# Optimization experiments

Measured on AMD Instinct MI355X. Metric: run time of the kernel, lower is better.

Reference implementation:

```python
import jax, jax.numpy as jnp
import numpy as np

N, E, G, B, L = 24576, 98304, 512, 512, 1000
F_IN, H1, C1, C2, HID = 5, 2, 64, 128, 256


def setup_inputs() -> dict:
    key = jax.random.key(0)
    ks = jax.random.split(key, 20)
    rn = lambda k, s: jax.random.normal(k, s, jnp.float32) * 0.1
    return {
        "x": jax.random.normal(ks[0], (N, F_IN), jnp.float32),
        "edge_index": jax.random.randint(ks[1], (2, E), 0, N),
        "batch": jnp.sort(jax.random.randint(ks[2], (N,), 0, G)),
        "protein_seq": jax.random.randint(ks[3], (B, L), 0, 22),
        "W1": rn(ks[4], (F_IN, H1 * C1)), "att_src1": rn(ks[5], (H1, C1)), "att_dst1": rn(ks[6], (H1, C1)), "b1": jnp.zeros((H1 * C1,), jnp.float32),
        "W2": rn(ks[7], (H1 * C1, C2)), "att_src2": rn(ks[8], (1, C2)), "att_dst2": rn(ks[9], (1, C2)), "b2": jnp.zeros((C2,), jnp.float32),
        "Wd": rn(ks[10], (C2, HID)), "bd": jnp.zeros((HID,), jnp.float32),
        "Pe": rn(ks[11], (22, 64)),
        "K1": rn(ks[12], (64, 64, 3)), "bk1": jnp.zeros((64,), jnp.float32),
        "K2": rn(ks[13], (128, 64, 5)), "bk2": jnp.zeros((128,), jnp.float32),
        "Wp": rn(ks[14], (128, HID)), "bp": jnp.zeros((HID,), jnp.float32),
        "Wf1": rn(ks[15], (2 * HID, 128)), "bf1": jnp.zeros((128,), jnp.float32),
        "Wf2": rn(ks[16], (128, 64)), "bf2": jnp.zeros((64,), jnp.float32),
        "Wo": rn(ks[17], (64, 1)), "bo": jnp.zeros((1,), jnp.float32),
    }


def _gat(x, edge_index, W, att_src, att_dst, b, heads, out_ch):
    """PyG GATConv: add self-loops, per-edge LeakyReLU(0.2) scores, segment softmax over dst."""
    n = x.shape[0]
    h = (x @ W).reshape(n, heads, out_ch)
    loop = jnp.arange(n)
    src = jnp.concatenate([edge_index[0], loop])
    dst = jnp.concatenate([edge_index[1], loop])
    a_s = jnp.sum(h * att_src[None], axis=-1)  # [n, H]
    a_d = jnp.sum(h * att_dst[None], axis=-1)
    e = jax.nn.leaky_relu(a_s[src] + a_d[dst], negative_slope=0.2)  # [E+n, H]
    m = jax.ops.segment_max(e, dst, num_segments=n)
    w = jnp.exp(e - m[dst])
    den = jax.ops.segment_sum(w, dst, num_segments=n)
    alpha = w / (den[dst] + 1e-16)
    out = jax.ops.segment_sum(h[src] * alpha[..., None], dst, num_segments=n)
    return out.reshape(n, heads * out_ch) + b


def _conv1d(x, k, pad):  # x: [B,C,L], k: [O,I,K]
    return jax.lax.conv_general_dilated(x, k, (1,), [(pad, pad)], dimension_numbers=("NCH", "OIH", "NCH"))


def reference(x, edge_index, batch, protein_seq, W1, att_src1, att_dst1, b1, W2, att_src2, att_dst2, b2, Wd, bd, Pe, K1, bk1, K2, bk2, Wp, bp, Wf1, bf1, Wf2, bf2, Wo, bo):
    # drug branch (GAT x2 + global mean pool)
    g = jax.nn.elu(_gat(x, edge_index, W1, att_src1, att_dst1, b1, H1, C1))
    g = jax.nn.elu(_gat(g, edge_index, W2, att_src2, att_dst2, b2, 1, C2))
    sums = jax.ops.segment_sum(g, batch, num_segments=G)
    cnt = jax.ops.segment_sum(jnp.ones((g.shape[0], 1), g.dtype), batch, num_segments=G)
    drug = jax.nn.relu(sums / jnp.maximum(cnt, 1.0) @ Wd + bd)
    # protein branch (embed -> conv1d x2 -> global max pool)
    pe = Pe[protein_seq].transpose(0, 2, 1)  # [B, 64, L]
    p = jax.nn.elu(_conv1d(pe, K1, 1) + bk1[None, :, None])
    p = jax.nn.elu(_conv1d(p, K2, 2) + bk2[None, :, None])
    prot = jax.nn.relu(jnp.max(p, axis=2) @ Wp + bp)
    # head
    h = jnp.concatenate([drug, prot], axis=1)
    h = jax.nn.relu(h @ Wf1 + bf1)
    h = jax.nn.relu(h @ Wf2 + bf2)
    return h @ Wo + bo
```

## Files before the change

kernel.cpp:

```cpp
#include <hip/hip_runtime.h>
#include <hip/hip_bf16.h>
#include <math.h>

#define NN 24576
#define NE 98304
#define ETOT (NE + NN)
#define NG 512
#define NB 512
#define LL 1000
#define TL 60
#define NTILE 17
#define PROT_BLKS (NB * NTILE)
#define CNT_BLKS (ETOT / 256)
#define AS1_BLKS (NN * 2 / 256)

typedef __attribute__((ext_vector_type(8))) short short8;
typedef __attribute__((ext_vector_type(4))) short short4v;
typedef __attribute__((ext_vector_type(4))) float f32x4;

__device__ inline short f2bf(float x) {
    union { __hip_bfloat16 b; short s; } u;
    u.b = __float2bfloat16(x);
    return u.s;
}

__device__ inline float bf2f(short s) {
    return __uint_as_float(((unsigned)(unsigned short)s) << 16);
}

__global__ void k_init_prep(int* deg, int* cursor, float* sums, float* cnt,
                            const float* K1, const float* K2, const float* W2, const float* Pe,
                            const float* W1, const float* as1c, const float* ad1c,
                            const float* as2c, const float* ad2c, const float* bk1,
                            short* Bswz2, short* Bh2, short* Bl2, float* M1,
                            float* wvec) {
    int bid = blockIdx.x, t = threadIdx.x;
    if (bid < 256) {
        int i = bid * 256 + t;
        if (i < NN) { deg[i] = 0; cursor[i] = 0; }
        if (i < NG * 128) sums[i] = 0.f;
        if (i < NG) cnt[i] = 0.f;
        return;
    }
    int idx = (bid - 256) * 256 + t;
    if (idx < 20) {
        int q = idx % 10, hd = q / 5, f = q % 5;
        const float* av = (idx < 10) ? as1c : ad1c;
        float s = 0.f;
        for (int c = 0; c < 64; c++) s += W1[f * 128 + hd * 64 + c] * av[hd * 64 + c];
        wvec[idx < 10 ? q : 10 + q] = s;
    }
    if (idx >= 32 && idx < 288) {
        int q = idx - 32;
        int kk = q & 127;
        const float* av = (q < 128) ? as2c : ad2c;
        float s = 0.f;
        for (int n2 = 0; n2 < 128; n2++) s += W2[kk * 128 + n2] * av[n2];
        wvec[idx] = s;
    }
    if (idx < 22 * 3 * 64) {
        int tok = idx / 192, r2 = idx % 192;
        int k = r2 >> 6, oc = r2 & 63;
        float s = (k == 1) ? bk1[oc] : 0.f;
        for (int ic = 0; ic < 64; ic++) s += K1[oc * 192 + ic * 3 + k] * Pe[tok * 64 + ic];
        M1[idx] = s;
    }
    if (idx < 320 * 128) {
        int j = idx & 7, lane = (idx >> 3) & 63, rest = idx >> 9;
        int nt = rest & 7, kb = rest >> 3;
        int k = kb * 32 + ((lane >> 4) << 3) + j;
        int n = nt * 16 + (lane & 15);
        int kk = k / 64, i = k % 64;
        Bswz2[idx] = f2bf(K2[n * 320 + i * 5 + kk]);
    }
    if (idx < 128 * 128) {
        int j = idx & 7, lane = (idx >> 3) & 63, rest = idx >> 9;
        int nt = rest & 7, kb = rest >> 3;
        int k = kb * 32 + ((lane >> 4) << 3) + j;
        int n = nt * 16 + (lane & 15);
        float v = W2[k * 128 + n];
        short hh = f2bf(v);
        Bh2[idx] = hh;
        Bl2[idx] = f2bf(v - bf2f(hh));
    }
}

#define SSTR 72
__global__ __launch_bounds__(256, 6) void k_prot_cnt_as1(
    const int* seq, const float* M1,
    const short* Bswz2, float* pmaxp,
    const int* ei, int* deg, const int* batch, float* cnt,
    const float* x, const float* wvec, float* rec) {
    int bid = blockIdx.x;
    int t = threadIdx.x;

    if (bid < CNT_BLKS) {
        int e = bid * 256 + t;
        int d = (e < NE) ? ei[NE + e] : e - NE;
        atomicAdd(&deg[d], 1);
        return;
    }
    if (bid < CNT_BLKS + AS1_BLKS) {
        int idx = (bid - CNT_BLKS) * 256 + t;
        int n = idx >> 1, hd = idx & 1;
        float xv[5];
        float s = 0.f, dv = 0.f;
#pragma unroll
        for (int f = 0; f < 5; f++) {
            xv[f] = x[n * 5 + f];
            s += xv[f] * wvec[hd * 5 + f];
            dv += xv[f] * wvec[10 + hd * 5 + f];
        }
        float* rr = &rec[n * 16];
        if (hd == 0) {
#pragma unroll
            for (int f = 0; f < 5; f++) rr[f] = xv[f];
            rr[5] = s; rr[7] = dv;
            atomicAdd(&cnt[batch[n]], 1.f);
        } else {
            rr[6] = s; rr[8] = dv;
        }
        return;
    }

    __shared__ __align__(16) short s1[68 * SSTR];

    int pb = bid - (CNT_BLKS + AS1_BLKS);
    int b = pb / NTILE;
    int tile = pb - b * NTILE;
    int t0 = tile * TL;

    if (t < 36) {
        *(short8*)&s1[64 * SSTR + t * 8] = (short8){0, 0, 0, 0, 0, 0, 0, 0};
    }

    {
        int q = t >> 2, c0 = (t & 3) << 4;
        int l = t0 - 2 + q;
        short tmp[16];
        if (l >= 0 && l < LL) {
            float v[16];
#pragma unroll
            for (int j = 0; j < 16; j++) v[j] = 0.f;
#pragma unroll
            for (int k = 0; k < 3; k++) {
                int lp = l - 1 + k;
                if (lp >= 0 && lp < LL) {
                    int tok = seq[b * LL + lp];
                    const float4* mr = (const float4*)&M1[tok * 192 + k * 64 + c0];
#pragma unroll
                    for (int j = 0; j < 4; j++) {
                        float4 mv = mr[j];
                        v[j * 4 + 0] += mv.x; v[j * 4 + 1] += mv.y;
                        v[j * 4 + 2] += mv.z; v[j * 4 + 3] += mv.w;
                    }
                }
            }
#pragma unroll
            for (int j = 0; j < 16; j++) {
                float xv = v[j];
                xv = xv > 0.f ? xv : __expf(xv) - 1.f;
                tmp[j] = f2bf(xv);
            }
        } else {
#pragma unroll
            for (int j = 0; j < 16; j++) tmp[j] = 0;
        }
        *(short8*)&s1[q * SSTR + c0] = *(short8*)&tmp[0];
        *(short8*)&s1[q * SSTR + c0 + 8] = *(short8*)&tmp[8];
    }
    __syncthreads();

    int wv = t >> 6, lane = t & 63;
    int ln15 = lane & 15, quad = lane >> 4;

    f32x4 acc2[4][2];
#pragma unroll
    for (int mi = 0; mi < 4; mi++)
#pragma unroll
        for (int ni = 0; ni < 2; ni++) acc2[mi][ni] = (f32x4){0.f, 0.f, 0.f, 0.f};
#pragma unroll
    for (int kb = 0; kb < 10; kb++) {
        int koff = kb * 32 + quad * 8;
        int kk = koff >> 6, i0 = koff & 63;
        short8 a[4], bb[2];
#pragma unroll
        for (int mi = 0; mi < 4; mi++)
            a[mi] = *(const short8*)&s1[(mi * 16 + ln15 + kk) * SSTR + i0];
#pragma unroll
        for (int ni = 0; ni < 2; ni++)
            bb[ni] = *(const short8*)&Bswz2[((kb * 8 + wv * 2 + ni) * 64 + lane) * 8];
#pragma unroll
        for (int mi = 0; mi < 4; mi++)
#pragma unroll
            for (int ni = 0; ni < 2; ni++)
                acc2[mi][ni] = __builtin_amdgcn_mfma_f32_16x16x32_bf16(a[mi], bb[ni], acc2[mi][ni], 0, 0, 0);
    }

#pragma unroll
    for (int ni = 0; ni < 2; ni++) {
        int col = (wv * 2 + ni) * 16 + ln15;
        float mx = -1e30f;
#pragma unroll
        for (int mi = 0; mi < 4; mi++) {
#pragma unroll
            for (int r = 0; r < 4; r++) {
                int p = mi * 16 + quad * 4 + r;
                if (p < TL && t0 + p < LL) mx = fmaxf(mx, acc2[mi][ni][r]);
            }
        }
        mx = fmaxf(mx, __shfl_xor(mx, 16, 64));
        mx = fmaxf(mx, __shfl_xor(mx, 32, 64));
        if (quad == 0) pmaxp[(b * NTILE + tile) * 128 + col] = mx;
    }
}

__global__ void k_scan1(const int* deg, int* excl, int* part) {
    __shared__ int s[256];
    int b = blockIdx.x, t = threadIdx.x, i = b * 256 + t;
    int v = deg[i];
    s[t] = v;
    __syncthreads();
    for (int o = 1; o < 256; o <<= 1) {
        int x = (t >= o) ? s[t - o] : 0;
        __syncthreads();
        s[t] += x;
        __syncthreads();
    }
    excl[i] = s[t] - v;
    if (t == 255) part[b] = s[t];
}

__global__ void k_scan23(const int* excl, const int* part, int* rowptr) {
    __shared__ int sp[96];
    __shared__ int pref;
    int b = blockIdx.x, t = threadIdx.x;
    if (t < 96) sp[t] = part[t];
    __syncthreads();
    if (t == 0) {
        int run = 0;
        for (int i = 0; i < b; i++) run += sp[i];
        pref = run;
    }
    __syncthreads();
    int i = b * 256 + t;
    rowptr[i] = excl[i] + pref;
    if (i == 0) rowptr[NN] = ETOT;
}

__global__ void k_scatter(const int* ei, const int* rowptr, int* cursor, int* colidx) {
    int e = blockIdx.x * 256 + threadIdx.x;
    if (e >= ETOT) return;
    int s, d;
    if (e < NE) { s = ei[e]; d = ei[NE + e]; }
    else { s = d = e - NE; }
    int pos = atomicAdd(&cursor[d], 1);
    colidx[rowptr[d] + pos] = s;
}

__global__ void k_agg2x(const int* rowptr, const int* colidx, const float* rec,
                        const float* W1, const float* b1, const float* wvec,
                        unsigned int* g1b, float* as2, float* ad2) {
    __shared__ float sW[640];
    __shared__ float sb1[128];
    __shared__ float swa[256];
    int t = threadIdx.x;
    for (int i = t; i < 640; i += 256) sW[i] = W1[i];
    if (t < 128) { sb1[t] = b1[t]; swa[t] = wvec[32 + t]; swa[128 + t] = wvec[160 + t]; }
    __syncthreads();

    int d = blockIdx.x * 16 + (t >> 4);
    int g = t & 15;
    int hd = (g < 5) ? 0 : 1;
    int f = (g < 5) ? g : g - 5;
    float adv = rec[d * 16 + 7 + hd];
    int p0 = rowptr[d], p1 = rowptr[d + 1];
    float den = 0.f, acc = 0.f;
    if (g < 10) {
        for (int pc = p0; pc < p1; pc += 4) {
            int sarr[4]; float ev[4], xv[4];
#pragma unroll
            for (int i = 0; i < 4; i++) {
                int pp = pc + i;
                sarr[i] = colidx[pp < p1 ? pp : p1 - 1];
            }
#pragma unroll
            for (int i = 0; i < 4; i++) {
                ev[i] = rec[sarr[i] * 16 + 5 + hd];
                xv[i] = rec[sarr[i] * 16 + f];
            }
#pragma unroll
            for (int i = 0; i < 4; i++) {
                if (pc + i < p1) {
                    float e = ev[i] + adv;
                    e = e >= 0.f ? e : 0.2f * e;
                    float w = __expf(e);
                    den += w;
                    acc += w * xv[i];
                }
            }
        }
    }
    float xn = acc / (den + 1e-16f);
    int gb = (t & 63) & ~15;
    int hcol = g >> 3;
    float xs[5];
#pragma unroll
    for (int f2 = 0; f2 < 5; f2++)
        xs[f2] = __shfl(xn, gb + hcol * 5 + f2, 64);
    float ps = 0.f, pd = 0.f;
    float g1v[8];
#pragma unroll
    for (int k = 0; k < 8; k++) {
        int col = g * 8 + k;
        float v = sb1[col];
#pragma unroll
        for (int f2 = 0; f2 < 5; f2++) v += xs[f2] * sW[f2 * 128 + col];
        v = v > 0.f ? v : __expf(v) - 1.f;
        g1v[k] = v;
        ps += v * swa[col];
        pd += v * swa[128 + col];
    }
    uint4 pk;
    pk.x = ((unsigned)(unsigned short)f2bf(g1v[1]) << 16) | (unsigned)(unsigned short)f2bf(g1v[0]);
    pk.y = ((unsigned)(unsigned short)f2bf(g1v[3]) << 16) | (unsigned)(unsigned short)f2bf(g1v[2]);
    pk.z = ((unsigned)(unsigned short)f2bf(g1v[5]) << 16) | (unsigned)(unsigned short)f2bf(g1v[4]);
    pk.w = ((unsigned)(unsigned short)f2bf(g1v[7]) << 16) | (unsigned)(unsigned short)f2bf(g1v[6]);
    *(uint4*)&g1b[d * 64 + g * 4] = pk;
#pragma unroll
    for (int msk = 1; msk < 16; msk <<= 1) {
        ps += __shfl_xor(ps, msk, 64);
        pd += __shfl_xor(pd, msk, 64);
    }
    if (g == 0) { as2[d] = ps; ad2[d] = pd; }
}

__global__ void k_agg1y(const int* rowptr, const int* colidx, const unsigned int* hb,
                        const float* as_, const float* ad_, float* yacc) {
    int t = threadIdx.x;
    int d = blockIdx.x * 4 + (t >> 6);
    int c = t & 63;
    float adv = ad_[d];
    int p0 = rowptr[d], p1 = rowptr[d + 1];
    float den = 0.f, acc0 = 0.f, acc1 = 0.f;
    for (int pc = p0; pc < p1; pc += 4) {
        int sarr[4]; float ev[4]; unsigned int hv[4];
#pragma unroll
        for (int i = 0; i < 4; i++) {
            int pp = pc + i;
            sarr[i] = colidx[pp < p1 ? pp : p1 - 1];
        }
#pragma unroll
        for (int i = 0; i < 4; i++) {
            ev[i] = as_[sarr[i]];
            hv[i] = hb[sarr[i] * 64 + c];
        }
#pragma unroll
        for (int i = 0; i < 4; i++) {
            if (pc + i < p1) {
                float e = ev[i] + adv;
                e = e >= 0.f ? e : 0.2f * e;
                float w = __expf(e);
                den += w;
                acc0 += w * __uint_as_float(hv[i] << 16);
                acc1 += w * __uint_as_float(hv[i] & 0xFFFF0000u);
            }
        }
    }
    float inv = 1.f / (den + 1e-16f);
    ((float2*)yacc)[d * 64 + c] = (float2){acc0 * inv, acc1 * inv};
}

#define ASTR 136
__global__ __launch_bounds__(256, 2) void k_g2mm(
    const float* yacc, const short* Bh, const short* Bl, const float* b2,
    const int* batch, float* sums) {
    __shared__ __align__(16) short Ah[64 * ASTR];
    __shared__ __align__(16) short Al[64 * ASTR];
    __shared__ int sb[64];
    int t = threadIdx.x;
    int m0 = blockIdx.x * 64;
    int wv = t >> 6, lane = t & 63;
    int ln15 = lane & 15, quad = lane >> 4;

    if (t < 64) sb[t] = batch[m0 + t];
    for (int i = t; i < 64 * 32; i += 256) {
        int row = i >> 5, c4 = (i & 31) * 4;
        float4 v = *(const float4*)&yacc[(m0 + row) * 128 + c4];
        short4v hi, lo;
        hi.x = f2bf(v.x); lo.x = f2bf(v.x - bf2f(hi.x));
        hi.y = f2bf(v.y); lo.y = f2bf(v.y - bf2f(hi.y));
        hi.z = f2bf(v.z); lo.z = f2bf(v.z - bf2f(hi.z));
        hi.w = f2bf(v.w); lo.w = f2bf(v.w - bf2f(hi.w));
        *(short4v*)&Ah[row * ASTR + c4] = hi;
        *(short4v*)&Al[row * ASTR + c4] = lo;
    }
    __syncthreads();

    f32x4 acc[8];
#pragma unroll
    for (int nt = 0; nt < 8; nt++) acc[nt] = (f32x4){0.f, 0.f, 0.f, 0.f};
    int arow = wv * 16 + ln15;
#pragma unroll
    for (int kb = 0; kb < 4; kb++) {
        int koff = kb * 32 + quad * 8;
        short8 a_hi = *(const short8*)&Ah[arow * ASTR + koff];
        short8 a_lo = *(const short8*)&Al[arow * ASTR + koff];
#pragma unroll
        for (int nt = 0; nt < 8; nt++) {
            short8 bh = *(const short8*)&Bh[((kb * 8 + nt) * 64 + lane) * 8];
            short8 bl = *(const short8*)&Bl[((kb * 8 + nt) * 64 + lane) * 8];
            acc[nt] = __builtin_amdgcn_mfma_f32_16x16x32_bf16(a_hi, bh, acc[nt], 0, 0, 0);
            acc[nt] = __builtin_amdgcn_mfma_f32_16x16x32_bf16(a_hi, bl, acc[nt], 0, 0, 0);
            acc[nt] = __builtin_amdgcn_mfma_f32_16x16x32_bf16(a_lo, bh, acc[nt], 0, 0, 0);
        }
    }
    int rbase = wv * 16 + quad * 4;
#pragma unroll
    for (int nt = 0; nt < 8; nt++) {
        int col = nt * 16 + ln15;
        float bias = b2[col];
        float run = 0.f;
        int cg = sb[rbase];
#pragma unroll
        for (int r = 0; r < 4; r++) {
            float v = acc[nt][r] + bias;
            v = v > 0.f ? v : __expf(v) - 1.f;
            int g = sb[rbase + r];
            if (g != cg) {
                atomicAdd(&sums[cg * 128 + col], run);
                run = 0.f; cg = g;
            }
            run += v;
        }
        atomicAdd(&sums[cg * 128 + col], run);
    }
}

__global__ __launch_bounds__(512) void k_tail(
    const float* pmaxp, const float* bk2, const float* Wp, const float* bp,
    const float* sums, const float* cnt, const float* Wd, const float* bd,
    const float* Wf1, const float* bf1, const float* Wf2, const float* bf2,
    const float* Wo, const float* bo, float* out) {
    __shared__ float spm[128];
    __shared__ float in2[512];
    __shared__ float part1[512];
    __shared__ float hh[128];
    __shared__ float part2[512];
    __shared__ float h2s[64];
    int g = blockIdx.x, t = threadIdx.x;

    if (t < 128) {
        float m = -1e30f;
#pragma unroll
        for (int tt = 0; tt < NTILE; tt++)
            m = fmaxf(m, pmaxp[(g * NTILE + tt) * 128 + t]);
        float v = m + bk2[t];
        spm[t] = v > 0.f ? v : __expf(v) - 1.f;
    }
    __syncthreads();

    if (t < 256) {
        float pacc = bp[t];
#pragma unroll 8
        for (int i = 0; i < 128; i++) pacc += spm[i] * Wp[i * 256 + t];
        in2[256 + t] = pacc > 0.f ? pacc : 0.f;
    } else {
        int o = t - 256;
        float c = cnt[g]; c = c < 1.f ? 1.f : c;
        float inv = 1.f / c;
        float dacc = bd[o];
#pragma unroll 8
        for (int i = 0; i < 128; i++) dacc += sums[g * 128 + i] * inv * Wd[i * 256 + o];
        in2[o] = dacc > 0.f ? dacc : 0.f;
    }
    __syncthreads();

    {
        int o = t >> 2, ks = t & 3;
        float p = 0.f;
        int c0 = ks * 128;
#pragma unroll 8
        for (int cc = c0; cc < c0 + 128; cc++) p += in2[cc] * Wf1[cc * 128 + o];
        part1[t] = p;
    }
    __syncthreads();
    if (t < 128) {
        float a = bf1[t] + part1[t * 4] + part1[t * 4 + 1] + part1[t * 4 + 2] + part1[t * 4 + 3];
        hh[t] = a > 0.f ? a : 0.f;
    }
    __syncthreads();

    {
        int o = t >> 3, ks = t & 7;
        float p = 0.f;
        int c0 = ks * 16;
#pragma unroll
        for (int cc = c0; cc < c0 + 16; cc++) p += hh[cc] * Wf2[cc * 64 + o];
        part2[t] = p;
    }
    __syncthreads();
    if (t < 64) {
        float a = bf2[t];
#pragma unroll
        for (int k = 0; k < 8; k++) a += part2[t * 8 + k];
        h2s[t] = a > 0.f ? a : 0.f;
    }
    __syncthreads();

    if (t < 64) {
        float p = h2s[t] * Wo[t];
#pragma unroll
        for (int off = 32; off > 0; off >>= 1) p += __shfl_down(p, off, 64);
        if (t == 0) out[g] = p + bo[0];
    }
}

extern "C" void kernel_launch(void* const* d_in, const int* in_sizes, int n_in,
                              void* d_out, int out_size, void* d_ws, size_t ws_size,
                              hipStream_t stream) {
    (void)in_sizes; (void)n_in; (void)out_size; (void)ws_size;
    const float* x   = (const float*)d_in[0];
    const int* ei    = (const int*)d_in[1];
    const int* batch = (const int*)d_in[2];
    const int* seq   = (const int*)d_in[3];
    const float* W1  = (const float*)d_in[4];
    const float* a_s1 = (const float*)d_in[5];
    const float* a_d1 = (const float*)d_in[6];
    const float* b1  = (const float*)d_in[7];
    const float* W2  = (const float*)d_in[8];
    const float* a_s2 = (const float*)d_in[9];
    const float* a_d2 = (const float*)d_in[10];
    const float* b2  = (const float*)d_in[11];
    const float* Wd  = (const float*)d_in[12];
    const float* bd  = (const float*)d_in[13];
    const float* Pe  = (const float*)d_in[14];
    const float* K1  = (const float*)d_in[15];
    const float* bk1 = (const float*)d_in[16];
    const float* K2  = (const float*)d_in[17];
    const float* bk2 = (const float*)d_in[18];
    const float* Wp  = (const float*)d_in[19];
    const float* bp  = (const float*)d_in[20];
    const float* Wf1 = (const float*)d_in[21];
    const float* bf1 = (const float*)d_in[22];
    const float* Wf2 = (const float*)d_in[23];
    const float* bf2 = (const float*)d_in[24];
    const float* Wo  = (const float*)d_in[25];
    const float* bo  = (const float*)d_in[26];
    float* out = (float*)d_out;

    float* w = (float*)d_ws;
    float* g1bf = w; w += NN * 64;
    float* yacc = w; w += NN * 128;
    float* as2  = w; w += NN;
    float* ad2  = w; w += NN;
    float* sums = w; w += NG * 128;
    float* cnt  = w; w += NG;
    float* pmaxp = w; w += NB * NTILE * 128;
    float* rec  = w; w += NN * 16;
    float* wvec = w; w += 512;
    short* Bswz2 = (short*)w; w += 320 * 128 / 2;
    short* Bh2  = (short*)w; w += 128 * 128 / 2;
    short* Bl2  = (short*)w; w += 128 * 128 / 2;
    float* M1   = w; w += 22 * 3 * 64;
    int* deg    = (int*)w; w += NN;
    int* cursor = (int*)w; w += NN;
    int* excl   = (int*)w; w += NN;
    int* part   = (int*)w; w += 128;
    int* rowptr = (int*)w; w += NN + 8;
    int* colidx = (int*)w; w += ETOT;

    unsigned int* g1b = (unsigned int*)g1bf;

    hipLaunchKernelGGL(k_init_prep, dim3(256 + 160), dim3(256), 0, stream,
                       deg, cursor, sums, cnt,
                       K1, K2, W2, Pe, W1, a_s1, a_d1, a_s2, a_d2, bk1,
                       Bswz2, Bh2, Bl2, M1, wvec);

    hipLaunchKernelGGL(k_prot_cnt_as1, dim3(CNT_BLKS + AS1_BLKS + PROT_BLKS), dim3(256), 0, stream,
                       seq, M1, Bswz2, pmaxp,
                       ei, deg, batch, cnt, x, wvec, rec);

    hipLaunchKernelGGL(k_scan1, dim3(NN / 256), dim3(256), 0, stream, deg, excl, part);
    hipLaunchKernelGGL(k_scan23, dim3(NN / 256), dim3(256), 0, stream, excl, part, rowptr);
    hipLaunchKernelGGL(k_scatter, dim3(ETOT / 256), dim3(256), 0, stream, ei, rowptr, cursor, colidx);

    hipLaunchKernelGGL(k_agg2x, dim3(NN / 16), dim3(256), 0, stream,
                       rowptr, colidx, rec, W1, b1, wvec, g1b, as2, ad2);

    hipLaunchKernelGGL(k_agg1y, dim3(NN / 4), dim3(256), 0, stream,
                       rowptr, colidx, g1b, as2, ad2, yacc);

    hipLaunchKernelGGL(k_g2mm, dim3(NN / 64), dim3(256), 0, stream,
                       yacc, Bh2, Bl2, b2, batch, sums);

    hipLaunchKernelGGL(k_tail, dim3(NG), dim3(512), 0, stream,
                       pmaxp, bk2, Wp, bp, sums, cnt, Wd, bd, Wf1, bf1, Wf2, bf2, Wo, bo, out);
}
```

Before: 282.6 us.

## Spread protein conv tiles across graph-build kernels and merge scan passes

Splits the 8704 protein conv tiles into four chunks and places them as extra blocks in the degree-count, scan, scatter and first-aggregation kernels. Graph CSR-build kernels have few blocks and leave the GPU underused, so the dense MFMA work is meant to fill those idle compute units. The two scan kernels are merged into one using an atomic counter spin-wait across the 96 scan blocks, which removes a launch and the excl buffer. The spin-wait can deadlock if the scan blocks are not all resident at once, and unroll 2 on the MFMA loop trades instruction count against scheduling freedom.

```diff
diff --git a/kernel.cpp b/kernel.cpp
--- a/kernel.cpp
+++ b/kernel.cpp
@@ -10,9 +10,17 @@
 #define LL 1000
 #define TL 60
 #define NTILE 17
-#define PROT_BLKS (NB * NTILE)
+#define PROT_TOT (NB * NTILE)
 #define CNT_BLKS (ETOT / 256)
 #define AS1_BLKS (NN * 2 / 256)
+#define P1_CNT 1792
+#define P2_CNT 1280
+#define P3_CNT 1536
+#define P4_CNT 4096
+#define P1_OFF 0
+#define P2_OFF (P1_CNT)
+#define P3_OFF (P1_CNT + P2_CNT)
+#define P4_OFF (P1_CNT + P2_CNT + P3_CNT)
 
 typedef __attribute__((ext_vector_type(8))) short short8;
 typedef __attribute__((ext_vector_type(4))) short short4v;
@@ -28,7 +36,101 @@
     return __uint_as_float(((unsigned)(unsigned short)s) << 16);
 }
 
-__global__ void k_init_prep(int* deg, int* cursor, float* sums, float* cnt,
+#define SSTR 72
+#define SMEM_BYTES 9792
+__device__ __forceinline__ void prot_body(int pb, int t, char* smem,
+        const int* seq, const float* M1, const short* Bswz2, float* pmaxp) {
+    short* s1 = (short*)smem;
+    int b = pb / NTILE;
+    int tile = pb - b * NTILE;
+    int t0 = tile * TL;
+
+    if (t < 36) {
+        *(short8*)&s1[64 * SSTR + t * 8] = (short8){0, 0, 0, 0, 0, 0, 0, 0};
+    }
+
+    {
+        int q = t >> 2, c0 = (t & 3) << 4;
+        int l = t0 - 2 + q;
+        short tmp[16];
+        if (l >= 0 && l < LL) {
+            float v[16];
+#pragma unroll
+            for (int j = 0; j < 16; j++) v[j] = 0.f;
+#pragma unroll
+            for (int k = 0; k < 3; k++) {
+                int lp = l - 1 + k;
+                if (lp >= 0 && lp < LL) {
+                    int tok = seq[b * LL + lp];
+                    const float4* mr = (const float4*)&M1[tok * 192 + k * 64 + c0];
+#pragma unroll
+                    for (int j = 0; j < 4; j++) {
+                        float4 mv = mr[j];
+                        v[j * 4 + 0] += mv.x; v[j * 4 + 1] += mv.y;
+                        v[j * 4 + 2] += mv.z; v[j * 4 + 3] += mv.w;
+                    }
+                }
+            }
+#pragma unroll
+            for (int j = 0; j < 16; j++) {
+                float xv = v[j];
+                xv = xv > 0.f ? xv : __expf(xv) - 1.f;
+                tmp[j] = f2bf(xv);
+            }
+        } else {
+#pragma unroll
+            for (int j = 0; j < 16; j++) tmp[j] = 0;
+        }
+        *(short8*)&s1[q * SSTR + c0] = *(short8*)&tmp[0];
+        *(short8*)&s1[q * SSTR + c0 + 8] = *(short8*)&tmp[8];
+    }
+    __syncthreads();
+
+    int wv = t >> 6, lane = t & 63;
+    int ln15 = lane & 15, quad = lane >> 4;
+
+    f32x4 acc2[4][2];
+#pragma unroll
+    for (int mi = 0; mi < 4; mi++)
+#pragma unroll
+        for (int ni = 0; ni < 2; ni++) acc2[mi][ni] = (f32x4){0.f, 0.f, 0.f, 0.f};
+#pragma unroll 2
+    for (int kb = 0; kb < 10; kb++) {
+        int koff = kb * 32 + quad * 8;
+        int kk = koff >> 6, i0 = koff & 63;
+        short8 a[4], bb[2];
+#pragma unroll
+        for (int mi = 0; mi < 4; mi++)
+            a[mi] = *(const short8*)&s1[(mi * 16 + ln15 + kk) * SSTR + i0];
+#pragma unroll
+        for (int ni = 0; ni < 2; ni++)
+            bb[ni] = *(const short8*)&Bswz2[((kb * 8 + wv * 2 + ni) * 64 + lane) * 8];
+#pragma unroll
+        for (int mi = 0; mi < 4; mi++)
+#pragma unroll
+            for (int ni = 0; ni < 2; ni++)
+                acc2[mi][ni] = __builtin_amdgcn_mfma_f32_16x16x32_bf16(a[mi], bb[ni], acc2[mi][ni], 0, 0, 0);
+    }
+
+#pragma unroll
+    for (int ni = 0; ni < 2; ni++) {
+        int col = (wv * 2 + ni) * 16 + ln15;
+        float mx = -1e30f;
+#pragma unroll
+        for (int mi = 0; mi < 4; mi++) {
+#pragma unroll
+            for (int r = 0; r < 4; r++) {
+                int p = mi * 16 + quad * 4 + r;
+                if (p < TL && t0 + p < LL) mx = fmaxf(mx, acc2[mi][ni][r]);
+            }
+        }
+        mx = fmaxf(mx, __shfl_xor(mx, 16, 64));
+        mx = fmaxf(mx, __shfl_xor(mx, 32, 64));
+        if (quad == 0) pmaxp[(b * NTILE + tile) * 128 + col] = mx;
+    }
+}
+
+__global__ void k_init_prep(int* deg, int* cursor, float* sums, float* cnt, int* ctr,
                             const float* K1, const float* K2, const float* W2, const float* Pe,
                             const float* W1, const float* as1c, const float* ad1c,
                             const float* as2c, const float* ad2c, const float* bk1,
@@ -40,6 +142,7 @@
         if (i < NN) { deg[i] = 0; cursor[i] = 0; }
         if (i < NG * 128) sums[i] = 0.f;
         if (i < NG) cnt[i] = 0.f;
+        if (i == 0) ctr[0] = 0;
         return;
     }
     int idx = (bid - 256) * 256 + t;
@@ -85,14 +188,12 @@
     }
 }
 
-#define SSTR 72
-__global__ __launch_bounds__(256, 6) void k_prot_cnt_as1(
-    const int* seq, const float* M1,
-    const short* Bswz2, float* pmaxp,
+__global__ __launch_bounds__(256, 6) void k_d2(
     const int* ei, int* deg, const int* batch, float* cnt,
-    const float* x, const float* wvec, float* rec) {
-    int bid = blockIdx.x;
-    int t = threadIdx.x;
+    const float* x, const float* wvec, float* rec,
+    const int* seq, const float* M1, const short* Bswz2, float* pmaxp) {
+    int bid = blockIdx.x, t = threadIdx.x;
+    __shared__ __align__(16) char smem[SMEM_BYTES];
 
     if (bid < CNT_BLKS) {
         int e = bid * 256 + t;
@@ -122,154 +223,89 @@
         }
         return;
     }
-
-    __shared__ __align__(16) short s1[68 * SSTR];
-
-    int pb = bid - (CNT_BLKS + AS1_BLKS);
-    int b = pb / NTILE;
-    int tile = pb - b * NTILE;
-    int t0 = tile * TL;
-
-    if (t < 36) {
-        *(short8*)&s1[64 * SSTR + t * 8] = (short8){0, 0, 0, 0, 0, 0, 0, 0};
-    }
-
-    {
-        int q = t >> 2, c0 = (t & 3) << 4;
-        int l = t0 - 2 + q;
-        short tmp[16];
-        if (l >= 0 && l < LL) {
-            float v[16];
-#pragma unroll
-            for (int j = 0; j < 16; j++) v[j] = 0.f;
-#pragma unroll
-            for (int k = 0; k < 3; k++) {
-                int lp = l - 1 + k;
-                if (lp >= 0 && lp < LL) {
-                    int tok = seq[b * LL + lp];
-                    const float4* mr = (const float4*)&M1[tok * 192 + k * 64 + c0];
-#pragma unroll
-                    for (int j = 0; j < 4; j++) {
-                        float4 mv = mr[j];
-                        v[j * 4 + 0] += mv.x; v[j * 4 + 1] += mv.y;
-                        v[j * 4 + 2] += mv.z; v[j * 4 + 3] += mv.w;
-                    }
-                }
-            }
-#pragma unroll
-            for (int j = 0; j < 16; j++) {
-                float xv = v[j];
-                xv = xv > 0.f ? xv : __expf(xv) - 1.f;
-                tmp[j] = f2bf(xv);
-            }
-        } else {
-#pragma unroll
-            for (int j = 0; j < 16; j++) tmp[j] = 0;
-        }
-        *(short8*)&s1[q * SSTR + c0] = *(short8*)&tmp[0];
-        *(short8*)&s1[q * SSTR + c0 + 8] = *(short8*)&tmp[8];
-    }
-    __syncthreads();
-
-    int wv = t >> 6, lane = t & 63;
-    int ln15 = lane & 15, quad = lane >> 4;
-
-    f32x4 acc2[4][2];
-#pragma unroll
-    for (int mi = 0; mi < 4; mi++)
-#pragma unroll
-        for (int ni = 0; ni < 2; ni++) acc2[mi][ni] = (f32x4){0.f, 0.f, 0.f, 0.f};
-#pragma unroll
-    for (int kb = 0; kb < 10; kb++) {
-        int koff = kb * 32 + quad * 8;
-        int kk = koff >> 6, i0 = koff & 63;
-        short8 a[4], bb[2];
-#pragma unroll
-        for (int mi = 0; mi < 4; mi++)
-            a[mi] = *(const short8*)&s1[(mi * 16 + ln15 + kk) * SSTR + i0];
-#pragma unroll
-        for (int ni = 0; ni < 2; ni++)
-            bb[ni] = *(const short8*)&Bswz2[((kb * 8 + wv * 2 + ni) * 64 + lane) * 8];
-#pragma unroll
-        for (int mi = 0; mi < 4; mi++)
-#pragma unroll
-            for (int ni = 0; ni < 2; ni++)
-                acc2[mi][ni] = __builtin_amdgcn_mfma_f32_16x16x32_bf16(a[mi], bb[ni], acc2[mi][ni], 0, 0, 0);
-    }
-
-#pragma unroll
-    for (int ni = 0; ni < 2; ni++) {
-        int col = (wv * 2 + ni) * 16 + ln15;
-        float mx = -1e30f;
-#pragma unroll
-        for (int mi = 0; mi < 4; mi++) {
-#pragma unroll
-            for (int r = 0; r < 4; r++) {
-                int p = mi * 16 + quad * 4 + r;
-                if (p < TL && t0 + p < LL) mx = fmaxf(mx, acc2[mi][ni][r]);
-            }
-        }
-        mx = fmaxf(mx, __shfl_xor(mx, 16, 64));
-        mx = fmaxf(mx, __shfl_xor(mx, 32, 64));
-        if (quad == 0) pmaxp[(b * NTILE + tile) * 128 + col] = mx;
-    }
-}
-
-__global__ void k_scan1(const int* deg, int* excl, int* part) {
-    __shared__ int s[256];
-    int b = blockIdx.x, t = threadIdx.x, i = b * 256 + t;
-    int v = deg[i];
-    s[t] = v;
-    __syncthreads();
-    for (int o = 1; o < 256; o <<= 1) {
-        int x = (t >= o) ? s[t - o] : 0;
+    prot_body(P1_OFF + (bid - (CNT_BLKS + AS1_BLKS)), t, smem, seq, M1, Bswz2, pmaxp);
+}
+
+__global__ __launch_bounds__(256, 6) void k_scan(
+    const int* deg, int* rowptr, int* part, int* ctr,
+    const int* seq, const float* M1, const short* Bswz2, float* pmaxp) {
+    int bid = blockIdx.x, t = threadIdx.x;
+    __shared__ __align__(16) char smem[SMEM_BYTES];
+
+    if (bid < 96) {
+        int* s = (int*)smem;
+        int* sp = (int*)(smem + 1024);
+        int b = bid, i = b * 256 + t;
+        int v = deg[i];
+        s[t] = v;
         __syncthreads();
-        s[t] += x;
+        for (int o = 1; o < 256; o <<= 1) {
+            int x2 = (t >= o) ? s[t - o] : 0;
+            __syncthreads();
+            s[t] += x2;
+            __syncthreads();
+        }
+        int excl = s[t] - v;
+        if (t == 255) {
+            part[b] = s[t];
+            __threadfence();
+            atomicAdd(ctr, 1);
+        }
+        if (t == 0) {
+            while (__hip_atomic_load(ctr, __ATOMIC_ACQUIRE, __HIP_MEMORY_SCOPE_AGENT) < 96) {}
+        }
         __syncthreads();
-    }
-    excl[i] = s[t] - v;
-    if (t == 255) part[b] = s[t];
-}
-
-__global__ void k_scan23(const int* excl, const int* part, int* rowptr) {
-    __shared__ int sp[96];
-    __shared__ int pref;
-    int b = blockIdx.x, t = threadIdx.x;
-    if (t < 96) sp[t] = part[t];
-    __syncthreads();
-    if (t == 0) {
-        int run = 0;
-        for (int i = 0; i < b; i++) run += sp[i];
-        pref = run;
-    }
-    __syncthreads();
-    int i = b * 256 + t;
-    rowptr[i] = excl[i] + pref;
-    if (i == 0) rowptr[NN] = ETOT;
-}
-
-__global__ void k_scatter(const int* ei, const int* rowptr, int* cursor, int* colidx) {
-    int e = blockIdx.x * 256 + threadIdx.x;
-    if (e >= ETOT) return;
-    int s, d;
-    if (e < NE) { s = ei[e]; d = ei[NE + e]; }
-    else { s = d = e - NE; }
-    int pos = atomicAdd(&cursor[d], 1);
-    colidx[rowptr[d] + pos] = s;
-}
-
-__global__ void k_agg2x(const int* rowptr, const int* colidx, const float* rec,
-                        const float* W1, const float* b1, const float* wvec,
-                        unsigned int* g1b, float* as2, float* ad2) {
-    __shared__ float sW[640];
-    __shared__ float sb1[128];
-    __shared__ float swa[256];
-    int t = threadIdx.x;
+        if (t < 96) sp[t] = __hip_atomic_load(&part[t], __ATOMIC_RELAXED, __HIP_MEMORY_SCOPE_AGENT);
+        __syncthreads();
+        int pref = 0;
+        for (int i2 = 0; i2 < b; i2++) pref += sp[i2];
+        rowptr[i] = excl + pref;
+        if (i == 0) rowptr[NN] = ETOT;
+        return;
+    }
+    prot_body(P2_OFF + (bid - 96), t, smem, seq, M1, Bswz2, pmaxp);
+}
+
+__global__ __launch_bounds__(256, 6) void k_scat(
+    const int* ei, const int* rowptr, int* cursor, int* colidx,
+    const int* seq, const float* M1, const short* Bswz2, float* pmaxp) {
+    int bid = blockIdx.x, t = threadIdx.x;
+    __shared__ __align__(16) char smem[SMEM_BYTES];
+
+    if (bid < CNT_BLKS) {
+        int e = bid * 256 + t;
+        int s, d;
+        if (e < NE) { s = ei[e]; d = ei[NE + e]; }
+        else { s = d = e - NE; }
+        int pos = atomicAdd(&cursor[d], 1);
+        colidx[rowptr[d] + pos] = s;
+        return;
+    }
+    prot_body(P3_OFF + (bid - CNT_BLKS), t, smem, seq, M1, Bswz2, pmaxp);
+}
+
+__global__ __launch_bounds__(256, 4) void k_mega(
+    const int* rowptr, const int* colidx, const float* rec,
+    const float* W1, const float* b1, const float* wvec,
+    unsigned int* g1b, float* as2, float* ad2,
+    const int* seq, const float* M1, const short* Bswz2, float* pmaxp) {
+    int bid = blockIdx.x, t = threadIdx.x;
+    __shared__ __align__(16) char smem[SMEM_BYTES];
+
+    int grp = bid / 11, r = bid - grp * 11;
+    if (r >= 3) {
+        prot_body(P4_OFF + grp * 8 + (r - 3), t, smem, seq, M1, Bswz2, pmaxp);
+        return;
+    }
+    int a = grp * 3 + r;
+    float* sW = (float*)smem;
+    float* sb1 = sW + 640;
+    float* swa = sb1 + 128;
     for (int i = t; i < 640; i += 256) sW[i] = W1[i];
     if (t < 128) { sb1[t] = b1[t]; swa[t] = wvec[32 + t]; swa[128 + t] = wvec[160 + t]; }
     __syncthreads();
 
-    int d = blockIdx.x * 16 + (t >> 4);
+    int d = a * 16 + (t >> 4);
     int g = t & 15;
     int hd = (g < 5) ? 0 : 1;
     int f = (g < 5) ? g : g - 5;
@@ -565,28 +601,33 @@
     float* M1   = w; w += 22 * 3 * 64;
     int* deg    = (int*)w; w += NN;
     int* cursor = (int*)w; w += NN;
-    int* excl   = (int*)w; w += NN;
     int* part   = (int*)w; w += 128;
+    int* ctr    = (int*)w; w += 8;
     int* rowptr = (int*)w; w += NN + 8;
     int* colidx = (int*)w; w += ETOT;
 
     unsigned int* g1b = (unsigned int*)g1bf;
 
     hipLaunchKernelGGL(k_init_prep, dim3(256 + 160), dim3(256), 0, stream,
-                       deg, cursor, sums, cnt,
+                       deg, cursor, sums, cnt, ctr,
                        K1, K2, W2, Pe, W1, a_s1, a_d1, a_s2, a_d2, bk1,
                        Bswz2, Bh2, Bl2, M1, wvec);
 
-    hipLaunchKernelGGL(k_prot_cnt_as1, dim3(CNT_BLKS + AS1_BLKS + PROT_BLKS), dim3(256), 0, stream,
-                       seq, M1, Bswz2, pmaxp,
-                       ei, deg, batch, cnt, x, wvec, rec);
-
-    hipLaunchKernelGGL(k_scan1, dim3(NN / 256), dim3(256), 0, stream, deg, excl, part);
-    hipLaunchKernelGGL(k_scan23, dim3(NN / 256), dim3(256), 0, stream, excl, part, rowptr);
-    hipLaunchKernelGGL(k_scatter, dim3(ETOT / 256), dim3(256), 0, stream, ei, rowptr, cursor, colidx);
-
-    hipLaunchKernelGGL(k_agg2x, dim3(NN / 16), dim3(256), 0, stream,
-                       rowptr, colidx, rec, W1, b1, wvec, g1b, as2, ad2);
+    hipLaunchKernelGGL(k_d2, dim3(CNT_BLKS + AS1_BLKS + P1_CNT), dim3(256), 0, stream,
+                       ei, deg, batch, cnt, x, wvec, rec,
+                       seq, M1, Bswz2, pmaxp);
+
+    hipLaunchKernelGGL(k_scan, dim3(96 + P2_CNT), dim3(256), 0, stream,
+                       deg, rowptr, part, ctr,
+                       seq, M1, Bswz2, pmaxp);
+
+    hipLaunchKernelGGL(k_scat, dim3(CNT_BLKS + P3_CNT), dim3(256), 0, stream,
+                       ei, rowptr, cursor, colidx,
+                       seq, M1, Bswz2, pmaxp);
+
+    hipLaunchKernelGGL(k_mega, dim3(512 * 11), dim3(256), 0, stream,
+                       rowptr, colidx, rec, W1, b1, wvec, g1b, as2, ad2,
+                       seq, M1, Bswz2, pmaxp);
 
     hipLaunchKernelGGL(k_agg1y, dim3(NN / 4), dim3(256), 0, stream,
                        rowptr, colidx, g1b, as2, ad2, yacc);
```

Result: slower. 290.1 us (+2.7%).
